# Kernel optimization log

Hardware: AMD Instinct MI355X
Metric: run time of the kernel (lower is better)

The kernel has to match this reference:

```python
import jax, jax.numpy as jnp
import numpy as np
import math

B, S, D, H = 2, 2048, 1024, 16
DK = D // H

def setup_inputs() -> dict:
    key = jax.random.key(0)
    ks = jax.random.split(key, 12)
    def xavier(k, shape):
        fan_in, fan_out = shape[1], shape[0]
        limit = math.sqrt(6.0 / (fan_in + fan_out))
        return jax.random.uniform(k, shape, jnp.float32, -limit, limit)
    inp = {
        'query': jax.random.normal(ks[0], (B, S, D), jnp.float32),
        'key':   jax.random.normal(ks[1], (B, S, D), jnp.float32),
        'value': jax.random.normal(ks[2], (B, S, D), jnp.float32),
        # causal mask, broadcast over heads: (B, 1, S, S), 1 = keep, 0 = mask
        'mask':  jnp.broadcast_to(jnp.tril(jnp.ones((S, S), jnp.int32)), (B, 1, S, S)),
        'Wq': xavier(ks[3], (D, D)), 'bq': jnp.zeros((D,), jnp.float32),
        'Wk': xavier(ks[4], (D, D)), 'bk': jnp.zeros((D,), jnp.float32),
        'Wv': xavier(ks[5], (D, D)), 'bv': jnp.zeros((D,), jnp.float32),
        'Wo': xavier(ks[6], (D, D)), 'bo': jnp.zeros((D,), jnp.float32),
    }
    return inp

def _split_heads(x):
    # (B, S, D) -> (B, H, S, DK)
    b, s, _ = x.shape
    return x.reshape(b, s, H, DK).transpose(0, 2, 1, 3)

def reference(query, key, value, mask, Wq, bq, Wk, bk, Wv, bv, Wo, bo):
    # torch nn.Linear: y = x @ W.T + b
    Q = _split_heads(query @ Wq.T + bq)   # (B,H,S,DK)
    K = _split_heads(key   @ Wk.T + bk)
    V = _split_heads(value @ Wv.T + bv)
    scores = jnp.einsum('bhqd,bhkd->bhqk', Q, K) / math.sqrt(DK)  # (B,H,S,S)
    scores = jnp.where(mask == 0, jnp.float32(-1e9), scores)
    attn = jax.nn.softmax(scores, axis=-1)  # dropout p=0 -> identity
    out = jnp.einsum('bhqk,bhkd->bhqd', attn, V)  # (B,H,S,DK)
    out = out.transpose(0, 2, 1, 3).reshape(query.shape[0], query.shape[1], D)
    return out @ Wo.T + bo
```

## Files before the change

### kernel.cpp

```cpp
#include <hip/hip_runtime.h>
#include <hip/hip_bf16.h>
#include <type_traits>


typedef __attribute__((ext_vector_type(8))) short short8;
typedef __attribute__((ext_vector_type(4))) short s16x4;
typedef __attribute__((ext_vector_type(4))) float floatx4;

__device__ __forceinline__ short f2bf(float x) {
    union { float f; unsigned u; } v; v.f = x;
    unsigned r = v.u + 0x7fffu + ((v.u >> 16) & 1u);
    return (short)(r >> 16);
}

__device__ __forceinline__ unsigned pk2bf(float a, float b) {
    union { __hip_bfloat162 h2; unsigned u; } cv;
    cv.h2 = __float22bfloat162_rn(make_float2(a, b));
    return cv.u;
}

__device__ __forceinline__ float fast_exp2(float x) {
#if __has_builtin(__builtin_amdgcn_exp2f)
    return __builtin_amdgcn_exp2f(x);
#else
    return __expf(x * 0.69314718056f);
#endif
}

typedef __attribute__((address_space(3))) short lds_short;
typedef __attribute__((address_space(1))) const short glb_short;
__device__ __forceinline__ void load_lds16(const void* g, void* l) {
    __builtin_amdgcn_global_load_lds((glb_short*)g, (lds_short*)l, 16, 0, 0);
}

__global__ __launch_bounds__(256) void cvt_all(
        const float* __restrict__ q, const float* __restrict__ k,
        const float* __restrict__ v,
        const float* __restrict__ wq, const float* __restrict__ wk,
        const float* __restrict__ wv, const float* __restrict__ wo,
        unsigned short* __restrict__ xq, unsigned short* __restrict__ xk,
        unsigned short* __restrict__ xv,
        unsigned short* __restrict__ wqb, unsigned short* __restrict__ wkb,
        unsigned short* __restrict__ wvb, unsigned short* __restrict__ wob) {
    const float* s; unsigned short* d;
    int bx = blockIdx.x;
    switch (blockIdx.y) {
        case 0: s = q; d = xq; break;
        case 1: s = k; d = xk; break;
        case 2: s = v; d = xv; break;
        default: {
            int wsel = bx >> 9; bx &= 511;
            s = (wsel == 0) ? wq : (wsel == 1) ? wk : (wsel == 2) ? wv : wo;
            d = (wsel == 0) ? wqb : (wsel == 1) ? wkb : (wsel == 2) ? wvb : wob;
        }
    }
    size_t i = ((size_t)bx * 256 + threadIdx.x) * 8;
    floatx4 a = *(const floatx4*)(s + i), b2 = *(const floatx4*)(s + i + 4);
    union { unsigned u[4]; short8 v8; } o;
    o.u[0] = pk2bf(a[0], a[1]);  o.u[1] = pk2bf(a[2], a[3]);
    o.u[2] = pk2bf(b2[0], b2[1]); o.u[3] = pk2bf(b2[2], b2[3]);
    *(short8*)(d + i) = o.v8;
}

__global__ __launch_bounds__(256, 6) void gemm_qkv(
        const unsigned short* __restrict__ Xq, const unsigned short* __restrict__ Xk,
        const unsigned short* __restrict__ Xv,
        const unsigned short* __restrict__ Wq, const unsigned short* __restrict__ Wk,
        const unsigned short* __restrict__ Wv,
        const float* __restrict__ bq, const float* __restrict__ bk,
        const float* __restrict__ bv,
        unsigned short* __restrict__ Qb, unsigned short* __restrict__ Kb,
        unsigned short* __restrict__ Vb) {
    constexpr int K = 1024, N = 1024;
    __shared__ short As[64 * 64];
    __shared__ short Bs[128 * 64];
    const int t = threadIdx.x;
    const int slot = blockIdx.x;
    const int p = (slot & 7) + 8 * (slot >> 6);
    const int nx = (slot >> 3) & 7;
    const int chunk = p >> 6, my = p & 63;
    const unsigned short* A = chunk == 0 ? Xq : chunk == 1 ? Xk : Xv;
    const unsigned short* W = chunk == 0 ? Wq : chunk == 1 ? Wk : Wv;
    const float* bias        = chunk == 0 ? bq : chunk == 1 ? bk : bv;
    unsigned short* Y        = chunk == 0 ? Qb : chunk == 1 ? Kb : Vb;
    const float scale = chunk == 0 ? 0.1803368801f : 1.0f;
    const int m0 = my * 64, n0 = nx * 128;
    const int lane = t & 63, w = t >> 6;
    const int l16 = lane & 15, quad = lane >> 4;
    const int srow8 = t >> 3, scs8 = t & 7;
    floatx4 acc[4][2] = {};

    for (int k0 = 0; k0 < K; k0 += 64) {
        __syncthreads();
        for (int i = 0; i < 2; i++) {
            const int row = i * 32 + srow8;
            const int cg = scs8 ^ (row & 7);
            load_lds16(A + (size_t)(m0 + row) * K + k0 + cg * 8, &As[i * 2048 + t * 8]);
        }
        for (int i = 0; i < 4; i++) {
            const int row = i * 32 + srow8;
            const int cg = scs8 ^ (row & 7);
            load_lds16(W + (size_t)(n0 + row) * K + k0 + cg * 8, &Bs[i * 2048 + t * 8]);
        }
        __syncthreads();

        for (int kc = 0; kc < 2; kc++) {
            short8 af[4], bf[2];
            for (int ms = 0; ms < 4; ms++) {
                const int row = ms * 16 + l16;
                af[ms] = *(short8*)&As[row * 64 + (((kc << 2) | quad) ^ (row & 7)) * 8];
            }
            for (int ns = 0; ns < 2; ns++) {
                const int row = w * 32 + ns * 16 + l16;
                bf[ns] = *(short8*)&Bs[row * 64 + (((kc << 2) | quad) ^ (row & 7)) * 8];
            }
            for (int ms = 0; ms < 4; ms++)
                for (int ns = 0; ns < 2; ns++)
                    acc[ms][ns] = __builtin_amdgcn_mfma_f32_16x16x32_bf16(
                            af[ms], bf[ns], acc[ms][ns], 0, 0, 0);
        }
    }

    if (chunk == 2) {
        for (int ms = 0; ms < 4; ms++)
            for (int ns = 0; ns < 2; ns++) {
                const int col = n0 + w * 32 + ns * 16 + l16;
                const float bb = bias[col];
                const int row0 = m0 + ms * 16 + quad * 4;
                const size_t dst = ((size_t)((row0 >> 11) * 16 + (col >> 6)) * 64
                                    + (col & 63)) * 2048 + (row0 & 2047);
                union { unsigned u[2]; s16x4 v4; } ow;
                ow.u[0] = pk2bf(acc[ms][ns][0] + bb, acc[ms][ns][1] + bb);
                ow.u[1] = pk2bf(acc[ms][ns][2] + bb, acc[ms][ns][3] + bb);
                *(s16x4*)(Y + dst) = ow.v4;
            }
    } else {
        for (int ms = 0; ms < 4; ms++)
            for (int ns = 0; ns < 2; ns++) {
                int col = n0 + w * 32 + ns * 16 + l16;
                float bb = bias[col];
                for (int r = 0; r < 4; r++) {
                    int row = m0 + ms * 16 + quad * 4 + r;
                    Y[(size_t)row * N + col] =
                        (unsigned short)f2bf((acc[ms][ns][r] + bb) * scale);
                }
            }
    }
}

__global__ __launch_bounds__(256, 4) void gemm_o(
        const unsigned short* __restrict__ A, const unsigned short* __restrict__ W,
        const float* __restrict__ bo, float* __restrict__ out) {
    constexpr int K = 1024, N = 1024;
    __shared__ short As[64 * 64];
    __shared__ short Bs[64 * 64];
    const int t = threadIdx.x;
    const int slot = blockIdx.x;
    const int p = (slot & 7) + 8 * (slot >> 7);
    const int nx = (slot >> 3) & 15;
    const int m0 = p * 64, n0 = nx * 64;
    const int lane = t & 63, w = t >> 6;
    const int l16 = lane & 15, quad = lane >> 4;
    const int wm = w >> 1, wn = w & 1;
    const int srow8 = t >> 3, scs8 = t & 7;
    floatx4 acc[2][2] = {};

    for (int k0 = 0; k0 < K; k0 += 64) {
        __syncthreads();
        for (int i = 0; i < 2; i++) {
            const int row = i * 32 + srow8;
            const int cg = scs8 ^ (row & 7);
            load_lds16(A + (size_t)(m0 + row) * K + k0 + cg * 8, &As[i * 2048 + t * 8]);
            load_lds16(W + (size_t)(n0 + row) * K + k0 + cg * 8, &Bs[i * 2048 + t * 8]);
        }
        __syncthreads();

        for (int kc = 0; kc < 2; kc++) {
            short8 af[2], bf[2];
            for (int ms = 0; ms < 2; ms++) {
                const int row = wm * 32 + ms * 16 + l16;
                af[ms] = *(short8*)&As[row * 64 + (((kc << 2) | quad) ^ (row & 7)) * 8];
            }
            for (int ns = 0; ns < 2; ns++) {
                const int row = wn * 32 + ns * 16 + l16;
                bf[ns] = *(short8*)&Bs[row * 64 + (((kc << 2) | quad) ^ (row & 7)) * 8];
            }
            for (int ms = 0; ms < 2; ms++)
                for (int ns = 0; ns < 2; ns++)
                    acc[ms][ns] = __builtin_amdgcn_mfma_f32_16x16x32_bf16(
                            af[ms], bf[ns], acc[ms][ns], 0, 0, 0);
        }
    }

    for (int ms = 0; ms < 2; ms++)
        for (int ns = 0; ns < 2; ns++) {
            int col = n0 + wn * 32 + ns * 16 + l16;
            float bb = bo[col];
            for (int r = 0; r < 4; r++) {
                int row = m0 + wm * 32 + ms * 16 + quad * 4 + r;
                out[(size_t)row * N + col] = acc[ms][ns][r] + bb;
            }
        }
}

__global__ __launch_bounds__(256) void attn_kernel(
        const unsigned short* __restrict__ Q, const unsigned short* __restrict__ Kp,
        const unsigned short* __restrict__ Vp, unsigned short* __restrict__ O) {
    __shared__ short Ks[64 * 64];
    __shared__ short Vt[64 * 64];
    __shared__ short Ps[4][16 * 64];
    const int t = threadIdx.x;
    const int bx = blockIdx.x;
    const int g = bx >> 8, c = bx & 255;
    const int dlt = c >> 5, bh = c & 31;
    const int unit = (g == 0) ? 31 - dlt : (g == 1) ? 23 - dlt
                   : (g == 2) ? 8 + dlt  : dlt;
    const int h = bh & 15, b = bh >> 4;
    const int q0 = unit * 64;
    const int lane = t & 63, w = t >> 6, l16 = lane & 15, quad = lane >> 4;
    const int krow = t >> 2, kcg = (t & 3) * 16;
    const int sc0 = (((t & 3) * 2)     ^ (krow & 7)) * 8;
    const int sc1 = (((t & 3) * 2 + 1) ^ (krow & 7)) * 8;

    short8 qf[2];
    {
        const size_t base = ((size_t)(b * 2048 + q0 + w * 16 + l16)) * 1024 + h * 64;
        qf[0] = *(const short8*)(Q + base + quad * 8);
        qf[1] = *(const short8*)(Q + base + 32 + quad * 8);
    }
    float l = 0.f;
    floatx4 o[4] = {};

    const size_t vtbase = ((size_t)((b * 16 + h) * 64 + krow)) * 2048;

    short8 ka, kb, va, vc;
    {
        const size_t kbse = ((size_t)(b * 2048 + krow)) * 1024 + h * 64 + kcg;
        ka = *(const short8*)(Kp + kbse);
        kb = *(const short8*)(Kp + kbse + 8);
        va = *(const short8*)(Vp + vtbase + kcg);
        vc = *(const short8*)(Vp + vtbase + kcg + 8);
    }

    for (int kv0 = 0; kv0 <= q0; kv0 += 64) {
        __syncthreads();
        *(short8*)&Ks[krow * 64 + sc0] = ka;
        *(short8*)&Ks[krow * 64 + sc1] = kb;
        *(short8*)&Vt[krow * 64 + sc0] = va;
        *(short8*)&Vt[krow * 64 + sc1] = vc;
        __syncthreads();

        if (kv0 < q0) {
            const size_t kbse = ((size_t)(b * 2048 + kv0 + 64 + krow)) * 1024 + h * 64 + kcg;
            ka = *(const short8*)(Kp + kbse);
            kb = *(const short8*)(Kp + kbse + 8);
            va = *(const short8*)(Vp + vtbase + kv0 + 64 + kcg);
            vc = *(const short8*)(Vp + vtbase + kv0 + 64 + kcg + 8);
        }

        floatx4 sv[4] = {};
        __builtin_amdgcn_s_setprio(1);
        for (int hh = 0; hh < 4; hh++)
            for (int kc = 0; kc < 2; kc++) {
                const int row = hh * 16 + l16;
                short8 kf = *(short8*)&Ks[row * 64 + (((kc << 2) | quad) ^ (row & 7)) * 8];
                sv[hh] = __builtin_amdgcn_mfma_f32_16x16x32_bf16(kf, qf[kc], sv[hh], 0, 0, 0);
            }
        __builtin_amdgcn_s_setprio(0);

        {
            const bool needmask = (kv0 + 63 > q0 + w * 16);
            const int qg = q0 + w * 16 + l16;
            float ls = 0.f;
            for (int hh = 0; hh < 4; hh++) {
                float pv[4];
                for (int r = 0; r < 4; r++) {
                    int kv = kv0 + hh * 16 + quad * 4 + r;
                    float e = fast_exp2(sv[hh][r]);
                    pv[r] = (needmask && kv > qg) ? 0.f : e;
                    ls += pv[r];
                }
                union { unsigned u[2]; s16x4 v4; } pw;
                pw.u[0] = pk2bf(pv[0], pv[1]); pw.u[1] = pk2bf(pv[2], pv[3]);
                *(s16x4*)&Ps[w][l16 * 64 + ((2 * hh + (quad >> 1)) ^ (l16 & 7)) * 8
                                + (quad & 1) * 4] = pw.v4;
            }
            ls += __shfl_xor(ls, 16);
            ls += __shfl_xor(ls, 32);
            l += ls;
        }

        short8 p0 = *(short8*)&Ps[w][l16 * 64 + (quad ^ (l16 & 7)) * 8];
        short8 p1 = *(short8*)&Ps[w][l16 * 64 + ((4 + quad) ^ (l16 & 7)) * 8];
        __builtin_amdgcn_s_setprio(1);
        for (int nc = 0; nc < 4; nc++) {
            const int row = nc * 16 + l16;
            short8 vf0 = *(short8*)&Vt[row * 64 + (quad ^ (row & 7)) * 8];
            short8 vf1 = *(short8*)&Vt[row * 64 + ((4 + quad) ^ (row & 7)) * 8];
            o[nc] = __builtin_amdgcn_mfma_f32_16x16x32_bf16(vf0, p0, o[nc], 0, 0, 0);
            o[nc] = __builtin_amdgcn_mfma_f32_16x16x32_bf16(vf1, p1, o[nc], 0, 0, 0);
        }
        __builtin_amdgcn_s_setprio(0);
    }

    const float rl = 1.f / l;
    const size_t orow = ((size_t)(b * 2048 + q0 + w * 16 + l16)) * 1024 + h * 64;
    for (int nc = 0; nc < 4; nc++) {
        union { unsigned u[2]; s16x4 v4; } ow;
        ow.u[0] = pk2bf(o[nc][0] * rl, o[nc][1] * rl);
        ow.u[1] = pk2bf(o[nc][2] * rl, o[nc][3] * rl);
        *(s16x4*)(O + orow + nc * 16 + quad * 4) = ow.v4;
    }
}

extern "C" void kernel_launch(void* const* d_in, const int* in_sizes, int n_in,
                              void* d_out, int out_size, void* d_ws, size_t ws_size,
                              hipStream_t stream) {
    const float* query = (const float*)d_in[0];
    const float* key   = (const float*)d_in[1];
    const float* value = (const float*)d_in[2];
    const float* Wq = (const float*)d_in[4];
    const float* bq = (const float*)d_in[5];
    const float* Wk = (const float*)d_in[6];
    const float* bk = (const float*)d_in[7];
    const float* Wv = (const float*)d_in[8];
    const float* bv = (const float*)d_in[9];
    const float* Wo = (const float*)d_in[10];
    const float* bo = (const float*)d_in[11];

    const size_t NE = (size_t)4096 * 1024;
    const size_t WE = (size_t)1024 * 1024;
    unsigned short* Xq  = (unsigned short*)d_ws;
    unsigned short* Xk  = Xq + NE;
    unsigned short* Xv  = Xk + NE;
    unsigned short* Qb  = Xv + NE;
    unsigned short* Kb  = Qb + NE;
    unsigned short* Vb  = Kb + NE;
    unsigned short* Ob  = Vb + NE;
    unsigned short* Wqb = Ob + NE;
    unsigned short* Wkb = Wqb + WE;
    unsigned short* Wvb = Wkb + WE;
    unsigned short* Wob = Wvb + WE;

    cvt_all<<<dim3(2048, 4), 256, 0, stream>>>(query, key, value, Wq, Wk, Wv, Wo,
                                               Xq, Xk, Xv, Wqb, Wkb, Wvb, Wob);
    gemm_qkv<<<dim3(1536), 256, 0, stream>>>(Xq, Xk, Xv, Wqb, Wkb, Wvb,
                                             bq, bk, bv, Qb, Kb, Vb);
    attn_kernel<<<dim3(1024), 256, 0, stream>>>(Qb, Kb, Vb, Ob);
    gemm_o<<<dim3(1024), 256, 0, stream>>>(Ob, Wob, bo, (float*)d_out);
}
```

Baseline: 220.6 us.

## Double the attention KV tile to 128 rows per synchronised iteration

The attention kernel now stages 128 keys and values per loop iteration instead of 64. Each thread loads four 16-byte chunks of K and of transposed V, and the V tile gets a wider XOR swizzle. The score MFMAs cover 8 row groups, and P·V runs in two 64-column halves, with the second half skipped on the final partial causal tile. The goal is to halve the number of barriers and global-load rounds per block and keep more loads in flight. The cost is more registers and LDS per block, plus wasted QK work on the half tile past the diagonal. A launch-bounds occupancy hint of 4 is also added.

Result: slower. 228.0 us (+3.4%).

```diff
diff --git a/kernel.cpp b/kernel.cpp
--- a/kernel.cpp
+++ b/kernel.cpp
@@ -203,11 +203,11 @@
         }
 }
 
-__global__ __launch_bounds__(256) void attn_kernel(
+__global__ __launch_bounds__(256, 4) void attn_kernel(
         const unsigned short* __restrict__ Q, const unsigned short* __restrict__ Kp,
         const unsigned short* __restrict__ Vp, unsigned short* __restrict__ O) {
-    __shared__ short Ks[64 * 64];
-    __shared__ short Vt[64 * 64];
+    __shared__ short Ks[128 * 64];
+    __shared__ short Vt[64 * 128];
     __shared__ short Ps[4][16 * 64];
     const int t = threadIdx.x;
     const int bx = blockIdx.x;
@@ -218,9 +218,13 @@
     const int h = bh & 15, b = bh >> 4;
     const int q0 = unit * 64;
     const int lane = t & 63, w = t >> 6, l16 = lane & 15, quad = lane >> 4;
-    const int krow = t >> 2, kcg = (t & 3) * 16;
-    const int sc0 = (((t & 3) * 2)     ^ (krow & 7)) * 8;
-    const int sc1 = (((t & 3) * 2 + 1) ^ (krow & 7)) * 8;
+    const int krow = t >> 1, kd0 = (t & 1) * 32;
+    const int vrow = t >> 2, vs0 = (t & 3) * 32;
+    int ksl[4], vsl[4];
+    for (int j = 0; j < 4; j++) {
+        ksl[j] = ((((t & 1) * 4 + j) ^ (krow & 7)) * 8);
+        vsl[j] = ((((t & 3) * 4 + j) ^ (vrow & 15)) * 8);
+    }
 
     short8 qf[2];
     {
@@ -231,36 +235,37 @@
     float l = 0.f;
     floatx4 o[4] = {};
 
-    const size_t vtbase = ((size_t)((b * 16 + h) * 64 + krow)) * 2048;
-
-    short8 ka, kb, va, vc;
+    const size_t vtb = ((size_t)((b * 16 + h) * 64 + vrow)) * 2048 + vs0;
+
+    short8 kr[4], vr[4];
     {
-        const size_t kbse = ((size_t)(b * 2048 + krow)) * 1024 + h * 64 + kcg;
-        ka = *(const short8*)(Kp + kbse);
-        kb = *(const short8*)(Kp + kbse + 8);
-        va = *(const short8*)(Vp + vtbase + kcg);
-        vc = *(const short8*)(Vp + vtbase + kcg + 8);
-    }
-
-    for (int kv0 = 0; kv0 <= q0; kv0 += 64) {
-        __syncthreads();
-        *(short8*)&Ks[krow * 64 + sc0] = ka;
-        *(short8*)&Ks[krow * 64 + sc1] = kb;
-        *(short8*)&Vt[krow * 64 + sc0] = va;
-        *(short8*)&Vt[krow * 64 + sc1] = vc;
-        __syncthreads();
-
-        if (kv0 < q0) {
-            const size_t kbse = ((size_t)(b * 2048 + kv0 + 64 + krow)) * 1024 + h * 64 + kcg;
-            ka = *(const short8*)(Kp + kbse);
-            kb = *(const short8*)(Kp + kbse + 8);
-            va = *(const short8*)(Vp + vtbase + kv0 + 64 + kcg);
-            vc = *(const short8*)(Vp + vtbase + kv0 + 64 + kcg + 8);
-        }
-
-        floatx4 sv[4] = {};
+        const size_t kbse = ((size_t)(b * 2048 + krow)) * 1024 + h * 64 + kd0;
+        for (int j = 0; j < 4; j++) {
+            kr[j] = *(const short8*)(Kp + kbse + 8 * j);
+            vr[j] = *(const short8*)(Vp + vtb + 8 * j);
+        }
+    }
+
+    for (int kv0 = 0; kv0 < q0 + 64; kv0 += 128) {
+        __syncthreads();
+        for (int j = 0; j < 4; j++) {
+            *(short8*)&Ks[krow * 64 + ksl[j]] = kr[j];
+            *(short8*)&Vt[vrow * 128 + vsl[j]] = vr[j];
+        }
+        __syncthreads();
+
+        if (kv0 + 128 < q0 + 64) {
+            const size_t kbse = ((size_t)(b * 2048 + kv0 + 128 + krow)) * 1024 + h * 64 + kd0;
+            for (int j = 0; j < 4; j++) {
+                kr[j] = *(const short8*)(Kp + kbse + 8 * j);
+                vr[j] = *(const short8*)(Vp + vtb + kv0 + 128 + 8 * j);
+            }
+        }
+
+        floatx4 sv[8];
+        for (int i = 0; i < 8; i++) sv[i] = (floatx4){0.f, 0.f, 0.f, 0.f};
         __builtin_amdgcn_s_setprio(1);
-        for (int hh = 0; hh < 4; hh++)
+        for (int hh = 0; hh < 8; hh++)
             for (int kc = 0; kc < 2; kc++) {
                 const int row = hh * 16 + l16;
                 short8 kf = *(short8*)&Ks[row * 64 + (((kc << 2) | quad) ^ (row & 7)) * 8];
@@ -268,10 +273,10 @@
             }
         __builtin_amdgcn_s_setprio(0);
 
+        float ls = 0.f;
         {
             const bool needmask = (kv0 + 63 > q0 + w * 16);
             const int qg = q0 + w * 16 + l16;
-            float ls = 0.f;
             for (int hh = 0; hh < 4; hh++) {
                 float pv[4];
                 for (int r = 0; r < 4; r++) {
@@ -285,22 +290,50 @@
                 *(s16x4*)&Ps[w][l16 * 64 + ((2 * hh + (quad >> 1)) ^ (l16 & 7)) * 8
                                 + (quad & 1) * 4] = pw.v4;
             }
-            ls += __shfl_xor(ls, 16);
-            ls += __shfl_xor(ls, 32);
-            l += ls;
-        }
-
-        short8 p0 = *(short8*)&Ps[w][l16 * 64 + (quad ^ (l16 & 7)) * 8];
-        short8 p1 = *(short8*)&Ps[w][l16 * 64 + ((4 + quad) ^ (l16 & 7)) * 8];
-        __builtin_amdgcn_s_setprio(1);
-        for (int nc = 0; nc < 4; nc++) {
-            const int row = nc * 16 + l16;
-            short8 vf0 = *(short8*)&Vt[row * 64 + (quad ^ (row & 7)) * 8];
-            short8 vf1 = *(short8*)&Vt[row * 64 + ((4 + quad) ^ (row & 7)) * 8];
-            o[nc] = __builtin_amdgcn_mfma_f32_16x16x32_bf16(vf0, p0, o[nc], 0, 0, 0);
-            o[nc] = __builtin_amdgcn_mfma_f32_16x16x32_bf16(vf1, p1, o[nc], 0, 0, 0);
-        }
-        __builtin_amdgcn_s_setprio(0);
+            short8 p0 = *(short8*)&Ps[w][l16 * 64 + (quad ^ (l16 & 7)) * 8];
+            short8 p1 = *(short8*)&Ps[w][l16 * 64 + ((4 + quad) ^ (l16 & 7)) * 8];
+            __builtin_amdgcn_s_setprio(1);
+            for (int nc = 0; nc < 4; nc++) {
+                const int row = nc * 16 + l16;
+                short8 vf0 = *(short8*)&Vt[row * 128 + ((quad) ^ (row & 15)) * 8];
+                short8 vf1 = *(short8*)&Vt[row * 128 + ((4 + quad) ^ (row & 15)) * 8];
+                o[nc] = __builtin_amdgcn_mfma_f32_16x16x32_bf16(vf0, p0, o[nc], 0, 0, 0);
+                o[nc] = __builtin_amdgcn_mfma_f32_16x16x32_bf16(vf1, p1, o[nc], 0, 0, 0);
+            }
+            __builtin_amdgcn_s_setprio(0);
+        }
+        if (kv0 < q0) {
+            const bool needmask = (kv0 + 127 > q0 + w * 16);
+            const int qg = q0 + w * 16 + l16;
+            for (int hh = 4; hh < 8; hh++) {
+                float pv[4];
+                for (int r = 0; r < 4; r++) {
+                    int kv = kv0 + hh * 16 + quad * 4 + r;
+                    float e = fast_exp2(sv[hh][r]);
+                    pv[r] = (needmask && kv > qg) ? 0.f : e;
+                    ls += pv[r];
+                }
+                union { unsigned u[2]; s16x4 v4; } pw;
+                pw.u[0] = pk2bf(pv[0], pv[1]); pw.u[1] = pk2bf(pv[2], pv[3]);
+                *(s16x4*)&Ps[w][l16 * 64 + ((2 * (hh - 4) + (quad >> 1)) ^ (l16 & 7)) * 8
+                                + (quad & 1) * 4] = pw.v4;
+            }
+            short8 p0 = *(short8*)&Ps[w][l16 * 64 + (quad ^ (l16 & 7)) * 8];
+            short8 p1 = *(short8*)&Ps[w][l16 * 64 + ((4 + quad) ^ (l16 & 7)) * 8];
+            __builtin_amdgcn_s_setprio(1);
+            for (int nc = 0; nc < 4; nc++) {
+                const int row = nc * 16 + l16;
+                short8 vf0 = *(short8*)&Vt[row * 128 + ((8 + quad) ^ (row & 15)) * 8];
+                short8 vf1 = *(short8*)&Vt[row * 128 + ((12 + quad) ^ (row & 15)) * 8];
+                o[nc] = __builtin_amdgcn_mfma_f32_16x16x32_bf16(vf0, p0, o[nc], 0, 0, 0);
+                o[nc] = __builtin_amdgcn_mfma_f32_16x16x32_bf16(vf1, p1, o[nc], 0, 0, 0);
+            }
+            __builtin_amdgcn_s_setprio(0);
+        }
+
+        ls += __shfl_xor(ls, 16);
+        ls += __shfl_xor(ls, 32);
+        l += ls;
     }
 
     const float rl = 1.f / l;
```

## Double-buffer K/V shared tiles in attention kernel to drop one barrier

Applied to the files above, without the earlier changes.

The K and V tiles in LDS are now double-buffered. Each iteration writes the next tile into the alternate buffer while computing on the current one, which leaves a single __syncthreads per iteration instead of two. Global prefetch now runs two tiles ahead. Shared memory use doubles to about 40KB per block, and launch_bounds now requests 4 blocks per CU, which may constrain registers.

After: 230.7 us. +4.6%, slower.

```diff
diff --git a/kernel.cpp b/kernel.cpp
--- a/kernel.cpp
+++ b/kernel.cpp
@@ -203,11 +203,11 @@
         }
 }
 
-__global__ __launch_bounds__(256) void attn_kernel(
+__global__ __launch_bounds__(256, 4) void attn_kernel(
         const unsigned short* __restrict__ Q, const unsigned short* __restrict__ Kp,
         const unsigned short* __restrict__ Vp, unsigned short* __restrict__ O) {
-    __shared__ short Ks[64 * 64];
-    __shared__ short Vt[64 * 64];
+    __shared__ short Ks[2][64 * 64];
+    __shared__ short Vt[2][64 * 64];
     __shared__ short Ps[4][16 * 64];
     const int t = threadIdx.x;
     const int bx = blockIdx.x;
@@ -241,21 +241,33 @@
         va = *(const short8*)(Vp + vtbase + kcg);
         vc = *(const short8*)(Vp + vtbase + kcg + 8);
     }
+    *(short8*)&Ks[0][krow * 64 + sc0] = ka;
+    *(short8*)&Ks[0][krow * 64 + sc1] = kb;
+    *(short8*)&Vt[0][krow * 64 + sc0] = va;
+    *(short8*)&Vt[0][krow * 64 + sc1] = vc;
+    if (q0 > 0) {
+        const size_t kbse = ((size_t)(b * 2048 + 64 + krow)) * 1024 + h * 64 + kcg;
+        ka = *(const short8*)(Kp + kbse);
+        kb = *(const short8*)(Kp + kbse + 8);
+        va = *(const short8*)(Vp + vtbase + 64 + kcg);
+        vc = *(const short8*)(Vp + vtbase + 64 + kcg + 8);
+    }
+    __syncthreads();
 
     for (int kv0 = 0; kv0 <= q0; kv0 += 64) {
-        __syncthreads();
-        *(short8*)&Ks[krow * 64 + sc0] = ka;
-        *(short8*)&Ks[krow * 64 + sc1] = kb;
-        *(short8*)&Vt[krow * 64 + sc0] = va;
-        *(short8*)&Vt[krow * 64 + sc1] = vc;
-        __syncthreads();
-
+        const int cur = (kv0 >> 6) & 1;
         if (kv0 < q0) {
-            const size_t kbse = ((size_t)(b * 2048 + kv0 + 64 + krow)) * 1024 + h * 64 + kcg;
+            *(short8*)&Ks[cur ^ 1][krow * 64 + sc0] = ka;
+            *(short8*)&Ks[cur ^ 1][krow * 64 + sc1] = kb;
+            *(short8*)&Vt[cur ^ 1][krow * 64 + sc0] = va;
+            *(short8*)&Vt[cur ^ 1][krow * 64 + sc1] = vc;
+        }
+        if (kv0 + 64 < q0) {
+            const size_t kbse = ((size_t)(b * 2048 + kv0 + 128 + krow)) * 1024 + h * 64 + kcg;
             ka = *(const short8*)(Kp + kbse);
             kb = *(const short8*)(Kp + kbse + 8);
-            va = *(const short8*)(Vp + vtbase + kv0 + 64 + kcg);
-            vc = *(const short8*)(Vp + vtbase + kv0 + 64 + kcg + 8);
+            va = *(const short8*)(Vp + vtbase + kv0 + 128 + kcg);
+            vc = *(const short8*)(Vp + vtbase + kv0 + 128 + kcg + 8);
         }
 
         floatx4 sv[4] = {};
@@ -263,7 +275,7 @@
         for (int hh = 0; hh < 4; hh++)
             for (int kc = 0; kc < 2; kc++) {
                 const int row = hh * 16 + l16;
-                short8 kf = *(short8*)&Ks[row * 64 + (((kc << 2) | quad) ^ (row & 7)) * 8];
+                short8 kf = *(short8*)&Ks[cur][row * 64 + (((kc << 2) | quad) ^ (row & 7)) * 8];
                 sv[hh] = __builtin_amdgcn_mfma_f32_16x16x32_bf16(kf, qf[kc], sv[hh], 0, 0, 0);
             }
         __builtin_amdgcn_s_setprio(0);
@@ -295,12 +307,14 @@
         __builtin_amdgcn_s_setprio(1);
         for (int nc = 0; nc < 4; nc++) {
             const int row = nc * 16 + l16;
-            short8 vf0 = *(short8*)&Vt[row * 64 + (quad ^ (row & 7)) * 8];
-            short8 vf1 = *(short8*)&Vt[row * 64 + ((4 + quad) ^ (row & 7)) * 8];
+            short8 vf0 = *(short8*)&Vt[cur][row * 64 + (quad ^ (row & 7)) * 8];
+            short8 vf1 = *(short8*)&Vt[cur][row * 64 + ((4 + quad) ^ (row & 7)) * 8];
             o[nc] = __builtin_amdgcn_mfma_f32_16x16x32_bf16(vf0, p0, o[nc], 0, 0, 0);
             o[nc] = __builtin_amdgcn_mfma_f32_16x16x32_bf16(vf1, p1, o[nc], 0, 0, 0);
         }
         __builtin_amdgcn_s_setprio(0);
+
+        __syncthreads();
     }
 
     const float rl = 1.f / l;
```
